# Kernel optimization log

Hardware: AMD Instinct MI355X
Metric: run time of the kernel (lower is better)

## Reference

```python
import jax, jax.numpy as jnp
import numpy as np
from jax import lax

NUM_EXPERTS = 5
K = 3


def setup_inputs() -> dict:
    key = jax.random.key(0)
    ks = jax.random.split(key, 16)
    B = 8192
    d_in, d_h = 32 * 10 * 10, 128

    def w(k, shape, fan_in):
        return jax.random.normal(k, shape, jnp.float32) / np.sqrt(fan_in)

    return {
        "x": jax.random.normal(ks[0], (B, 1, 28, 28), jnp.float32),
        # conv feature extractor: 28 -> conv5 -> 24 -> pool2 -> 12 -> conv3 -> 10
        "conv1_w": w(ks[1], (16, 1, 5, 5), 25),
        "conv1_b": jnp.zeros((16,), jnp.float32),
        "conv2_w": w(ks[2], (32, 16, 3, 3), 16 * 9),
        "conv2_b": jnp.zeros((32,), jnp.float32),
        # top-k gate
        "gate_w": w(ks[3], (d_in, NUM_EXPERTS), d_in),
        "gate_b": jnp.zeros((NUM_EXPERTS,), jnp.float32),
        # 5 experts: Linear(3200,128)-Tanh-Linear(128,128)-Tanh, stacked on axis 0
        "e1_w": w(ks[4], (NUM_EXPERTS, d_in, d_h), d_in),
        "e1_b": jnp.zeros((NUM_EXPERTS, d_h), jnp.float32),
        "e2_w": w(ks[5], (NUM_EXPERTS, d_h, d_h), d_h),
        "e2_b": jnp.zeros((NUM_EXPERTS, d_h), jnp.float32),
        # softmax head
        "sm_w": w(ks[6], (d_h, 10), d_h),
        "sm_b": jnp.zeros((10,), jnp.float32),
    }


def _conv_features(x, c1w, c1b, c2w, c2b):
    dn = ("NCHW", "OIHW", "NCHW")
    h = lax.conv_general_dilated(x, c1w, (1, 1), "VALID", dimension_numbers=dn)
    h = jax.nn.relu(h + c1b[None, :, None, None])          # [B,16,24,24]
    h = lax.reduce_window(h, -jnp.inf, lax.max, (1, 1, 2, 2), (1, 1, 2, 2), "VALID")  # [B,16,12,12]
    h = lax.conv_general_dilated(h, c2w, (1, 1), "VALID", dimension_numbers=dn)
    h = jax.nn.relu(h + c2b[None, :, None, None])          # [B,32,10,10]
    return h.reshape(h.shape[0], -1)                       # [B,3200]


def reference(x, conv1_w, conv1_b, conv2_w, conv2_b, gate_w, gate_b,
              e1_w, e1_b, e2_w, e2_b, sm_w, sm_b):
    h = _conv_features(x, conv1_w, conv1_b, conv2_w, conv2_b)  # [B, 3200]
    B = h.shape[0]

    # token-choice top-K gating over NUM_EXPERTS experts
    probs = jax.nn.softmax(h @ gate_w + gate_b, axis=-1)       # [B, E]
    topv, topi = lax.top_k(probs, K)                           # [B, K]
    topv = topv / jnp.sum(topv, axis=-1, keepdims=True)        # renormalize
    w_full = jnp.zeros((B, NUM_EXPERTS), h.dtype).at[
        jnp.arange(B)[:, None], topi].set(topv)                # [B, E] sparse combine weights

    # expert MLPs (small, computed densely and masked by gate weights)
    h1 = jnp.tanh(jnp.einsum("bd,edh->ebh", h, e1_w) + e1_b[:, None, :])   # [E,B,128]
    h2 = jnp.tanh(jnp.einsum("ebh,ehk->ebk", h1, e2_w) + e2_b[:, None, :])  # [E,B,128]
    moe_out = jnp.einsum("be,ebk->bk", w_full, h2)             # weighted sum combine, [B,128]

    logits = moe_out @ sm_w + sm_b                             # [B,10]
    return jax.nn.softmax(logits, axis=1)
```

## Files before the change

### kernel.cpp

```cpp
#include <hip/hip_runtime.h>
#include <hip/hip_bf16.h>
#include <hip/hip_fp16.h>

#define NB 8192
#define D_IN 3200
#define D_H 128
#define NE 5

typedef _Float16 f16x8 __attribute__((ext_vector_type(8)));
typedef _Float16 f16x4 __attribute__((ext_vector_type(4)));
typedef float f32x4 __attribute__((ext_vector_type(4)));

__device__ __forceinline__ void gload16(const _Float16* g, _Float16* l) {
    __builtin_amdgcn_global_load_lds(
        (const __attribute__((address_space(1))) void*)g,
        (__attribute__((address_space(3))) void*)l, 16, 0, 0);
}

__device__ __forceinline__ unsigned pack_hl(float v) {
    _Float16 vh = (_Float16)v;
    _Float16 vl = (_Float16)(v - (float)vh);
    unsigned short uh, ul;
    __builtin_memcpy(&uh, &vh, 2);
    __builtin_memcpy(&ul, &vl, 2);
    return (unsigned)uh | ((unsigned)ul << 16);
}

__global__ __launch_bounds__(256) void k_prep(const float* __restrict__ gw,
                                              const float* __restrict__ c2w,
                                              const float* __restrict__ c1w,
                                              float* __restrict__ gwC,
                                              _Float16* __restrict__ wpk,
                                              int* __restrict__ cnt) {
    int i = blockIdx.x * 256 + threadIdx.x;
    if (i < 16000) {
        int e = i / 3200, rem = i - e * 3200;
        int o = rem >> 5, co = rem & 31;
        gwC[i] = gw[(co * 100 + o) * 5 + e];
    } else if (i < 21120) {
        int j = i - 16000;
        int co = j / 160, k = j - co * 160;
        int s = k >> 4, ci = k & 15;
        float v = (s == 9) ? 0.f : c2w[(co * 16 + ci) * 9 + s];
        _Float16 vh = (_Float16)v;
        wpk[j] = vh;
        wpk[5120 + j] = (_Float16)(v - (float)vh);
    } else if (i < 21760) {
        int j = i - 21120;
        int c = (j * 1639) >> 16;
        int k = j - c * 40;
        float v = (k < 25) ? c1w[c * 25 + k] : 0.f;
        _Float16 vh = (_Float16)v;
        wpk[10240 + j] = vh;
        wpk[10880 + j] = (_Float16)(v - (float)vh);
    }
    if (blockIdx.x == 0 && threadIdx.x < NE) cnt[threadIdx.x] = 0;
}

#define PCL_S 24
__global__ __launch_bounds__(256, 4) void k_feat(
    const float* __restrict__ x, const float* __restrict__ c1b,
    const float* __restrict__ c2b,
    const float* __restrict__ gwC, const float* __restrict__ gb,
    const _Float16* __restrict__ wpk,
    const float* __restrict__ e1w, _Float16* __restrict__ wT,
    const float* __restrict__ e2w, _Float16* __restrict__ e2T,
    _Float16* __restrict__ h16, float* __restrict__ wfull)
{
    __shared__ union {
        struct {
            __align__(16) _Float16 b2h[5120];
            __align__(16) _Float16 b2l[5120];
            __align__(16) _Float16 b1h[640];
            __align__(16) _Float16 b1l[640];
            __align__(16) unsigned xs_hl[784];
            __align__(16) _Float16 pclh[144 * PCL_S];
            __align__(16) _Float16 pcll[144 * PCL_S];
            float red[32];
        } f;
        float tile[64 * 65];
    } S;
    int bid = blockIdx.x;
    int t = threadIdx.x;

    if (bid < 520) {
        if (bid < 500) {
            int e = bid / 100, rem = bid - e * 100;
            int k0 = (rem >> 1) * 64, n0 = (rem & 1) * 64;
            const float* src = e1w + (size_t)e * D_IN * D_H;
            _Float16* dst = wT + (size_t)e * D_H * D_IN;
            for (int i = 0; i < 16; ++i) {
                int idx = t + i * 256;
                int kr = idx >> 6, nc = idx & 63;
                S.tile[kr * 65 + nc] = src[(size_t)(k0 + kr) * D_H + n0 + nc];
            }
            __syncthreads();
            for (int i = 0; i < 16; ++i) {
                int idx = t + i * 256;
                int nr = idx >> 6, kc = idx & 63;
                dst[(size_t)(n0 + nr) * D_IN + k0 + kc] = (_Float16)S.tile[kc * 65 + nr];
            }
        } else {
            int idx2 = bid - 500;
            int e = idx2 >> 2, rem = idx2 & 3;
            int k0 = (rem >> 1) * 64, n0 = (rem & 1) * 64;
            const float* src = e2w + (size_t)e * D_H * D_H;
            _Float16* dst = e2T + (size_t)e * D_H * D_H;
            for (int i = 0; i < 16; ++i) {
                int idx = t + i * 256;
                int kr = idx >> 6, nc = idx & 63;
                S.tile[kr * 65 + nc] = src[(size_t)(k0 + kr) * D_H + n0 + nc];
            }
            __syncthreads();
            for (int i = 0; i < 16; ++i) {
                int idx = t + i * 256;
                int nr = idx >> 6, kc = idx & 63;
                dst[(size_t)(n0 + nr) * D_H + k0 + kc] = (_Float16)S.tile[kc * 65 + nr];
            }
        }
        return;
    }

    int b = bid - 520;
    int lane = t & 63, wv = t >> 6;
    int quad = lane >> 4, l16 = lane & 15;

    {
        _Float16* ldst = S.f.b2h;
        #pragma unroll
        for (int it = 0; it < 6; ++it) {
            int ci = t + it * 256;
            if (ci < 1440)
                gload16(wpk + ci * 8, ldst + (it * 256 + wv * 64) * 8);
        }
    }
    for (int i = t; i < 784; i += 256)
        S.f.xs_hl[i] = pack_hl(x[(size_t)b * 784 + i]);
    __syncthreads();

    {
        f16x8 b1hf = *(const f16x8*)&S.f.b1h[l16 * 40 + quad * 8];
        f16x8 b1lf = *(const f16x8*)&S.f.b1l[l16 * 40 + quad * 8];
        float bias1 = c1b[l16];
        int offw[8];
        #pragma unroll
        for (int j = 0; j < 8; ++j) {
            int k = quad * 8 + j; if (k > 24) k = 24;
            int uu = (k * 205) >> 10;
            offw[j] = k + 23 * uu;
        }
        int s_ = l16 & 3, qof = l16 >> 2;
        int dy = s_ >> 1, dx = s_ & 1;
        for (int T = wv * 9; T < wv * 9 + 9; ++T) {
            int q = T * 4 + qof;
            int qy = (q * 683) >> 13, qx = q - qy * 12;
            int base = (2 * qy + dy) * 28 + 2 * qx + dx;
            unsigned w[8];
            #pragma unroll
            for (int j = 0; j < 8; ++j) w[j] = S.f.xs_hl[base + offw[j]];
            union { f16x8 v; unsigned u[4]; } ah, al;
            #pragma unroll
            for (int jj = 0; jj < 4; ++jj) {
                ah.u[jj] = __builtin_amdgcn_perm(w[2 * jj + 1], w[2 * jj], 0x05040100u);
                al.u[jj] = __builtin_amdgcn_perm(w[2 * jj + 1], w[2 * jj], 0x07060302u);
            }
            f32x4 a1 = (f32x4){0.f, 0.f, 0.f, 0.f};
            a1 = __builtin_amdgcn_mfma_f32_16x16x32_f16(ah.v, b1hf, a1, 0, 0, 0);
            a1 = __builtin_amdgcn_mfma_f32_16x16x32_f16(ah.v, b1lf, a1, 0, 0, 0);
            a1 = __builtin_amdgcn_mfma_f32_16x16x32_f16(al.v, b1hf, a1, 0, 0, 0);
            float pv = fmaxf(fmaxf(a1[0], a1[1]), fmaxf(a1[2], a1[3]));
            pv = fmaxf(pv + bias1, 0.f);
            int pos = T * 4 + quad;
            _Float16 vh = (_Float16)pv;
            S.f.pclh[pos * PCL_S + l16] = vh;
            S.f.pcll[pos * PCL_S + l16] = (_Float16)(pv - (float)vh);
        }
    }
    __syncthreads();

    float part[5] = {0, 0, 0, 0, 0};
    int quadh = quad >> 1, quadl = quad & 1;
    const int offA[5] = {0, 2, 13, 24, 26};
    const int offB[5] = {1, 12, 14, 25, 0};
    {
        int nt = wv & 1;
        int co = nt * 16 + l16;
        f16x8 bh[5], bl[5];
        #pragma unroll
        for (int kc = 0; kc < 5; ++kc) {
            bh[kc] = *(const f16x8*)&S.f.b2h[co * 160 + kc * 32 + quad * 8];
            bl[kc] = *(const f16x8*)&S.f.b2l[co * 160 + kc * 32 + quad * 8];
        }
        float bco = c2b[co];
        for (int mt = wv >> 1; mt < 7; mt += 2) {
            int o_a = mt * 16 + l16;
            int o_cl = o_a < 100 ? o_a : 99;
            int pb = (o_cl / 10) * 12 + (o_cl % 10);
            f32x4 acc = (f32x4){0.f, 0.f, 0.f, 0.f};
            #pragma unroll
            for (int kc = 0; kc < 5; ++kc) {
                int off = quadh ? offB[kc] : offA[kc];
                f16x8 ah = *(const f16x8*)&S.f.pclh[(pb + off) * PCL_S + quadl * 8];
                f16x8 al = *(const f16x8*)&S.f.pcll[(pb + off) * PCL_S + quadl * 8];
                acc = __builtin_amdgcn_mfma_f32_16x16x32_f16(ah, bh[kc], acc, 0, 0, 0);
                acc = __builtin_amdgcn_mfma_f32_16x16x32_f16(ah, bl[kc], acc, 0, 0, 0);
                acc = __builtin_amdgcn_mfma_f32_16x16x32_f16(al, bh[kc], acc, 0, 0, 0);
            }
            if (mt < 6 || quad == 0) {
                int o0 = mt * 16 + quad * 4;
                f16x4 st;
                #pragma unroll
                for (int r = 0; r < 4; ++r) {
                    float hv = fmaxf(acc[r] + bco, 0.f);
                    st[r] = (_Float16)hv;
                    #pragma unroll
                    for (int e = 0; e < 5; ++e)
                        part[e] += hv * gwC[e * 3200 + (o0 + r) * 32 + co];
                }
                *(f16x4*)&h16[(size_t)b * D_IN + co * 100 + o0] = st;
            }
        }
    }

    #pragma unroll
    for (int e = 0; e < 5; ++e) {
        float v = part[e];
        for (int off = 32; off > 0; off >>= 1) v += __shfl_down(v, off, 64);
        if (lane == 0) S.f.red[wv * 8 + e] = v;
    }
    __syncthreads();
    if (t == 0) {
        float lg[5], p[5];
        float mx = -1e30f;
        for (int e = 0; e < 5; ++e) {
            lg[e] = S.f.red[e] + S.f.red[8 + e] + S.f.red[16 + e] + S.f.red[24 + e] + gb[e];
            mx = fmaxf(mx, lg[e]);
        }
        float sum = 0.f;
        for (int e = 0; e < 5; ++e) { p[e] = expf(lg[e] - mx); sum += p[e]; }
        for (int e = 0; e < 5; ++e) p[e] /= sum;
        bool used[5] = {false, false, false, false, false};
        float out5[5] = {0, 0, 0, 0, 0};
        int ti[3]; float tv[3]; float tsum = 0.f;
        for (int jj = 0; jj < 3; ++jj) {
            int best = 0; float bv = -1.f;
            for (int e = 0; e < 5; ++e)
                if (!used[e] && p[e] > bv) { bv = p[e]; best = e; }
            used[best] = true; ti[jj] = best; tv[jj] = bv; tsum += bv;
        }
        for (int jj = 0; jj < 3; ++jj) out5[ti[jj]] = tv[jj] / tsum;
        for (int e = 0; e < 5; ++e) wfull[b * 5 + e] = out5[e];
    }
}

__global__ __launch_bounds__(256) void k_compact(
    const float* __restrict__ wfull, int* __restrict__ cnt, int* __restrict__ lists)
{
    int tok = blockIdx.x * 256 + threadIdx.x;
    int lane = threadIdx.x & 63;
    float w[5];
    #pragma unroll
    for (int e = 0; e < 5; ++e) w[e] = wfull[(size_t)tok * 5 + e];
    #pragma unroll
    for (int e = 0; e < 5; ++e) {
        bool sel = w[e] > 0.f;
        unsigned long long mask = __ballot(sel);
        int leader = __ffsll((long long)mask) - 1;
        int base = 0;
        if (lane == leader) base = atomicAdd(&cnt[e], __popcll(mask));
        base = __shfl(base, leader, 64);
        if (sel) {
            int pos = base + __popcll(mask & ((1ull << lane) - 1ull));
            lists[e * NB + pos] = tok;
        }
    }
}

#define H1S 136
union __align__(16) SLds {
    struct { _Float16 As0[2048], As1[2048], Bs0[4096], Bs1[4096]; } p[2];
    struct {
        __align__(16) _Float16 h1s[64 * H1S];
        __align__(16) _Float16 e2ws[128 * H1S];
    } q;
};

__global__ __launch_bounds__(256, 3) void k_e1e2(
    const _Float16* __restrict__ h16, const _Float16* __restrict__ wT,
    const _Float16* __restrict__ e2T,
    const float* __restrict__ e1b, const float* __restrict__ e2b,
    const float* __restrict__ smw,
    const float* __restrict__ wfull, const int* __restrict__ cnt,
    const int* __restrict__ lists, float* __restrict__ logits)
{
    __shared__ SLds u;
    __shared__ float wfl[64];
    __shared__ int rows[64];
    int bid = blockIdx.x;
    int e = bid >> 7;
    int mt = bid & 127;
    int cnt_e = cnt[e];
    int m0 = mt * 64;
    if (m0 >= cnt_e) return;
    int t = threadIdx.x;
    int lane = t & 63, wv = t >> 6;
    int waveM = wv >> 1, waveN = wv & 1;
    int quad = lane >> 4, l16 = lane & 15;
    if (t < 64) {
        int r = m0 + t;
        int row = (r < cnt_e) ? lists[e * NB + r] : lists[e * NB];
        rows[t] = row;
        wfl[t] = (r < cnt_e) ? wfull[(size_t)row * 5 + e] : 0.f;
    }
    __syncthreads();

    const _Float16* bbase = wT + (size_t)e * (D_H * D_IN);
    int srow = t >> 2;
    int scol = (t & 3) * 8;
    const _Float16* aptr = h16 + (size_t)rows[srow] * D_IN + scol;
    const _Float16* bptr0 = bbase + (size_t)srow * D_IN + scol;
    const _Float16* bptr1 = bbase + (size_t)(64 + srow) * D_IN + scol;
    f32x4 acc[2][4];
    #pragma unroll
    for (int i = 0; i < 2; ++i)
        #pragma unroll
        for (int j = 0; j < 4; ++j) acc[i][j] = (f32x4){0.f, 0.f, 0.f, 0.f};

    _Float16* bufc = (_Float16*)&u.p[0];
    _Float16* bufn = (_Float16*)&u.p[1];
    #define STAGE(base, kk)                                           \
        do {                                                          \
            gload16(aptr  + (kk),        (base) + 0    + wv * 512);   \
            gload16(aptr  + (kk) + 32,   (base) + 2048 + wv * 512);   \
            gload16(bptr0 + (kk),        (base) + 4096 + wv * 512);   \
            gload16(bptr0 + (kk) + 32,   (base) + 8192 + wv * 512);   \
            gload16(bptr1 + (kk),        (base) + 4096 + 2048 + wv * 512); \
            gload16(bptr1 + (kk) + 32,   (base) + 8192 + 2048 + wv * 512); \
        } while (0)

    STAGE(bufc, 0);
    const int NT = D_IN / 64;
    for (int it = 0; it < NT; ++it) {
        if (it + 1 < NT) {
            STAGE(bufn, (it + 1) * 64);
            asm volatile("s_waitcnt vmcnt(6)" ::: "memory");
        } else {
            asm volatile("s_waitcnt vmcnt(0)" ::: "memory");
        }
        __builtin_amdgcn_s_barrier();
        __builtin_amdgcn_sched_barrier(0);
        #pragma unroll
        for (int ch = 0; ch < 2; ++ch) {
            const _Float16* Ab = bufc + (ch ? 2048 : 0);
            const _Float16* Bb = bufc + 4096 + (ch ? 4096 : 0);
            f16x8 af[2], bf[4];
            #pragma unroll
            for (int ms = 0; ms < 2; ++ms)
                af[ms] = *(const f16x8*)&Ab[(waveM * 32 + ms * 16 + l16) * 32 + quad * 8];
            #pragma unroll
            for (int ns = 0; ns < 4; ++ns)
                bf[ns] = *(const f16x8*)&Bb[(waveN * 64 + ns * 16 + l16) * 32 + quad * 8];
            #pragma unroll
            for (int ms = 0; ms < 2; ++ms)
                #pragma unroll
                for (int ns = 0; ns < 4; ++ns)
                    acc[ms][ns] = __builtin_amdgcn_mfma_f32_16x16x32_f16(af[ms], bf[ns], acc[ms][ns], 0, 0, 0);
        }
        __builtin_amdgcn_s_barrier();
        _Float16* tmp = bufc; bufc = bufn; bufn = tmp;
    }
    #undef STAGE

    #pragma unroll
    for (int ms = 0; ms < 2; ++ms) {
        int rbase = waveM * 32 + ms * 16 + quad * 4;
        #pragma unroll
        for (int ns = 0; ns < 4; ++ns) {
            int n = waveN * 64 + ns * 16 + l16;
            float bias = e1b[e * D_H + n];
            #pragma unroll
            for (int r = 0; r < 4; ++r)
                u.q.h1s[(rbase + r) * H1S + n] = (_Float16)tanhf(acc[ms][ns][r] + bias);
        }
    }
    __syncthreads();

    {
        int rr = t >> 1, cc = (t & 1) * 64;
        const _Float16* src = e2T + (size_t)e * (D_H * D_H) + (size_t)rr * D_H + cc;
        #pragma unroll
        for (int i = 0; i < 8; ++i)
            *(uint4*)&u.q.e2ws[rr * H1S + cc + i * 8] = *(const uint4*)(src + i * 8);
    }
    __syncthreads();

    f32x4 acc2[2][4];
    #pragma unroll
    for (int i = 0; i < 2; ++i)
        #pragma unroll
        for (int j = 0; j < 4; ++j) acc2[i][j] = (f32x4){0.f, 0.f, 0.f, 0.f};
    #pragma unroll
    for (int kc = 0; kc < 4; ++kc) {
        f16x8 a2[2], b2[4];
        #pragma unroll
        for (int ms = 0; ms < 2; ++ms)
            a2[ms] = *(const f16x8*)&u.q.h1s[(waveM * 32 + ms * 16 + l16) * H1S + kc * 32 + quad * 8];
        #pragma unroll
        for (int ns = 0; ns < 4; ++ns)
            b2[ns] = *(const f16x8*)&u.q.e2ws[(waveN * 64 + ns * 16 + l16) * H1S + kc * 32 + quad * 8];
        #pragma unroll
        for (int ms = 0; ms < 2; ++ms)
            #pragma unroll
            for (int ns = 0; ns < 4; ++ns)
                acc2[ms][ns] = __builtin_amdgcn_mfma_f32_16x16x32_f16(a2[ms], b2[ns], acc2[ms][ns], 0, 0, 0);
    }
    __syncthreads();

    _Float16* smwT = u.q.e2ws;
    for (int i = t; i < 2048; i += 256) {
        int n = i >> 7, k = i & 127;
        smwT[i] = (_Float16)(n < 10 ? smw[k * 10 + n] : 0.f);
    }
    #pragma unroll
    for (int ms = 0; ms < 2; ++ms) {
        int rbase = waveM * 32 + ms * 16 + quad * 4;
        #pragma unroll
        for (int ns = 0; ns < 4; ++ns) {
            int n = waveN * 64 + ns * 16 + l16;
            float bias = e2b[e * D_H + n];
            #pragma unroll
            for (int r = 0; r < 4; ++r) {
                int lrow = rbase + r;
                u.q.h1s[lrow * H1S + n] = (_Float16)(wfl[lrow] * tanhf(acc2[ms][ns][r] + bias));
            }
        }
    }
    __syncthreads();

    {
        f32x4 acc3 = (f32x4){0.f, 0.f, 0.f, 0.f};
        #pragma unroll
        for (int kc = 0; kc < 4; ++kc) {
            f16x8 a3 = *(const f16x8*)&u.q.h1s[(wv * 16 + l16) * H1S + kc * 32 + quad * 8];
            f16x8 b3 = *(const f16x8*)&smwT[l16 * 128 + kc * 32 + quad * 8];
            acc3 = __builtin_amdgcn_mfma_f32_16x16x32_f16(a3, b3, acc3, 0, 0, 0);
        }
        if (l16 < 10) {
            #pragma unroll
            for (int r = 0; r < 4; ++r) {
                int row = wv * 16 + quad * 4 + r;
                unsafeAtomicAdd(&logits[(size_t)rows[row] * 10 + l16], acc3[r]);
            }
        }
    }
}

__global__ __launch_bounds__(256) void k_smax(
    const float* __restrict__ logits, const float* __restrict__ smb,
    float* __restrict__ out)
{
    int r = blockIdx.x * 256 + threadIdx.x;
    float lg[10];
    float mx = -1e30f;
    #pragma unroll
    for (int c = 0; c < 10; ++c) {
        lg[c] = logits[(size_t)r * 10 + c] + smb[c];
        mx = fmaxf(mx, lg[c]);
    }
    float s = 0.f;
    #pragma unroll
    for (int c = 0; c < 10; ++c) { lg[c] = expf(lg[c] - mx); s += lg[c]; }
    float inv = 1.f / s;
    #pragma unroll
    for (int c = 0; c < 10; ++c) out[(size_t)r * 10 + c] = lg[c] * inv;
}

extern "C" void kernel_launch(void* const* d_in, const int* in_sizes, int n_in,
                              void* d_out, int out_size, void* d_ws, size_t ws_size,
                              hipStream_t stream)
{
    const float* x   = (const float*)d_in[0];
    const float* c1w = (const float*)d_in[1];
    const float* c1b = (const float*)d_in[2];
    const float* c2w = (const float*)d_in[3];
    const float* c2b = (const float*)d_in[4];
    const float* gw  = (const float*)d_in[5];
    const float* gb  = (const float*)d_in[6];
    const float* e1w = (const float*)d_in[7];
    const float* e1b = (const float*)d_in[8];
    const float* e2w = (const float*)d_in[9];
    const float* e2b = (const float*)d_in[10];
    const float* smw = (const float*)d_in[11];
    const float* smb = (const float*)d_in[12];
    float* out = (float*)d_out;

    char* ws = (char*)d_ws;
    size_t off = 0;
    auto alloc = [&](size_t bytes) {
        void* p = ws + off;
        off += (bytes + 255) & ~(size_t)255;
        return p;
    };
    _Float16* h16 = (_Float16*)alloc((size_t)NB * D_IN * 2);
    _Float16* wT  = (_Float16*)alloc((size_t)NE * D_H * D_IN * 2);
    _Float16* e2T = (_Float16*)alloc((size_t)NE * D_H * D_H * 2);
    float* wfull  = (float*)alloc((size_t)NB * NE * 4);
    float* logits = (float*)alloc((size_t)NB * 10 * 4);
    float* gwC    = (float*)alloc((size_t)NE * D_IN * 4);
    _Float16* wpk = (_Float16*)alloc((size_t)11520 * 2);
    int* cnt      = (int*)alloc(NE * 4);
    int* lists    = (int*)alloc((size_t)NE * NB * 4);

    hipMemsetAsync(logits, 0, (size_t)NB * 10 * 4, stream);
    k_prep<<<dim3(85), 256, 0, stream>>>(gw, c2w, c1w, gwC, wpk, cnt);
    k_feat<<<dim3(520 + NB), 256, 0, stream>>>(x, c1b, c2b, gwC, gb, wpk,
                                               e1w, wT, e2w, e2T, h16, wfull);
    k_compact<<<dim3(NB / 256), 256, 0, stream>>>(wfull, cnt, lists);
    k_e1e2<<<dim3(128 * NE), 256, 0, stream>>>(h16, wT, e2T, e1b, e2b, smw,
                                               wfull, cnt, lists, logits);
    k_smax<<<dim3(NB / 256), 256, 0, stream>>>(logits, smb, out);
}
```

Before: 264.1 us.

## Pad conv2 LDS weights, interleave gate weights per expert, vectorize input staging

Gate weights are repacked into an 8-wide interleaved layout so each output element reads its five expert gate weights with one vector load plus one scalar load, instead of five strided scalar loads. The conv2 weight rows in LDS are padded from 160 to 168 halves to reduce bank conflicts. Conv1 weights are now read from global memory rather than staged in LDS, which shrinks the LDS copy. The input image is loaded as float4 and packed four values per thread. In exchange the gate-weight buffer grows and conv1 weights now come through the cache instead of LDS.

```diff
diff --git a/kernel.cpp b/kernel.cpp
--- a/kernel.cpp
+++ b/kernel.cpp
@@ -29,30 +29,30 @@
 __global__ __launch_bounds__(256) void k_prep(const float* __restrict__ gw,
                                               const float* __restrict__ c2w,
                                               const float* __restrict__ c1w,
-                                              float* __restrict__ gwC,
+                                              float* __restrict__ gwC8,
                                               _Float16* __restrict__ wpk,
                                               int* __restrict__ cnt) {
     int i = blockIdx.x * 256 + threadIdx.x;
-    if (i < 16000) {
-        int e = i / 3200, rem = i - e * 3200;
-        int o = rem >> 5, co = rem & 31;
-        gwC[i] = gw[(co * 100 + o) * 5 + e];
-    } else if (i < 21120) {
-        int j = i - 16000;
+    if (i < 25600) {
+        int idx = i >> 3, e = i & 7;
+        int o = idx >> 5, co = idx & 31;
+        gwC8[i] = (e < 5) ? gw[(co * 100 + o) * 5 + e] : 0.f;
+    } else if (i < 30720) {
+        int j = i - 25600;
         int co = j / 160, k = j - co * 160;
         int s = k >> 4, ci = k & 15;
         float v = (s == 9) ? 0.f : c2w[(co * 16 + ci) * 9 + s];
         _Float16 vh = (_Float16)v;
-        wpk[j] = vh;
-        wpk[5120 + j] = (_Float16)(v - (float)vh);
-    } else if (i < 21760) {
-        int j = i - 21120;
+        wpk[co * 168 + k] = vh;
+        wpk[5376 + co * 168 + k] = (_Float16)(v - (float)vh);
+    } else if (i < 31360) {
+        int j = i - 30720;
         int c = (j * 1639) >> 16;
         int k = j - c * 40;
         float v = (k < 25) ? c1w[c * 25 + k] : 0.f;
         _Float16 vh = (_Float16)v;
-        wpk[10240 + j] = vh;
-        wpk[10880 + j] = (_Float16)(v - (float)vh);
+        wpk[10752 + j] = vh;
+        wpk[11392 + j] = (_Float16)(v - (float)vh);
     }
     if (blockIdx.x == 0 && threadIdx.x < NE) cnt[threadIdx.x] = 0;
 }
@@ -61,7 +61,7 @@
 __global__ __launch_bounds__(256, 4) void k_feat(
     const float* __restrict__ x, const float* __restrict__ c1b,
     const float* __restrict__ c2b,
-    const float* __restrict__ gwC, const float* __restrict__ gb,
+    const float* __restrict__ gwC8, const float* __restrict__ gb,
     const _Float16* __restrict__ wpk,
     const float* __restrict__ e1w, _Float16* __restrict__ wT,
     const float* __restrict__ e2w, _Float16* __restrict__ e2T,
@@ -69,10 +69,8 @@
 {
     __shared__ union {
         struct {
-            __align__(16) _Float16 b2h[5120];
-            __align__(16) _Float16 b2l[5120];
-            __align__(16) _Float16 b1h[640];
-            __align__(16) _Float16 b1l[640];
+            __align__(16) _Float16 b2h[5376];
+            __align__(16) _Float16 b2l[5376];
             __align__(16) unsigned xs_hl[784];
             __align__(16) _Float16 pclh[144 * PCL_S];
             __align__(16) _Float16 pcll[144 * PCL_S];
@@ -130,17 +128,22 @@
         #pragma unroll
         for (int it = 0; it < 6; ++it) {
             int ci = t + it * 256;
-            if (ci < 1440)
+            if (ci < 1344)
                 gload16(wpk + ci * 8, ldst + (it * 256 + wv * 64) * 8);
         }
     }
-    for (int i = t; i < 784; i += 256)
-        S.f.xs_hl[i] = pack_hl(x[(size_t)b * 784 + i]);
+    if (t < 196) {
+        float4 v4 = *(const float4*)&x[(size_t)b * 784 + t * 4];
+        uint4 pk;
+        pk.x = pack_hl(v4.x); pk.y = pack_hl(v4.y);
+        pk.z = pack_hl(v4.z); pk.w = pack_hl(v4.w);
+        *(uint4*)&S.f.xs_hl[t * 4] = pk;
+    }
     __syncthreads();
 
     {
-        f16x8 b1hf = *(const f16x8*)&S.f.b1h[l16 * 40 + quad * 8];
-        f16x8 b1lf = *(const f16x8*)&S.f.b1l[l16 * 40 + quad * 8];
+        f16x8 b1hf = *(const f16x8*)&wpk[10752 + l16 * 40 + quad * 8];
+        f16x8 b1lf = *(const f16x8*)&wpk[11392 + l16 * 40 + quad * 8];
         float bias1 = c1b[l16];
         int offw[8];
         #pragma unroll
@@ -188,8 +191,8 @@
         f16x8 bh[5], bl[5];
         #pragma unroll
         for (int kc = 0; kc < 5; ++kc) {
-            bh[kc] = *(const f16x8*)&S.f.b2h[co * 160 + kc * 32 + quad * 8];
-            bl[kc] = *(const f16x8*)&S.f.b2l[co * 160 + kc * 32 + quad * 8];
+            bh[kc] = *(const f16x8*)&S.f.b2h[co * 168 + kc * 32 + quad * 8];
+            bl[kc] = *(const f16x8*)&S.f.b2l[co * 168 + kc * 32 + quad * 8];
         }
         float bco = c2b[co];
         for (int mt = wv >> 1; mt < 7; mt += 2) {
@@ -213,9 +216,13 @@
                 for (int r = 0; r < 4; ++r) {
                     float hv = fmaxf(acc[r] + bco, 0.f);
                     st[r] = (_Float16)hv;
-                    #pragma unroll
-                    for (int e = 0; e < 5; ++e)
-                        part[e] += hv * gwC[e * 3200 + (o0 + r) * 32 + co];
+                    int idx = (o0 + r) * 32 + co;
+                    const f32x4 g0 = *(const f32x4*)&gwC8[(size_t)idx * 8];
+                    part[0] += hv * g0[0];
+                    part[1] += hv * g0[1];
+                    part[2] += hv * g0[2];
+                    part[3] += hv * g0[3];
+                    part[4] += hv * gwC8[(size_t)idx * 8 + 4];
                 }
                 *(f16x4*)&h16[(size_t)b * D_IN + co * 100 + o0] = st;
             }
@@ -506,14 +513,14 @@
     _Float16* e2T = (_Float16*)alloc((size_t)NE * D_H * D_H * 2);
     float* wfull  = (float*)alloc((size_t)NB * NE * 4);
     float* logits = (float*)alloc((size_t)NB * 10 * 4);
-    float* gwC    = (float*)alloc((size_t)NE * D_IN * 4);
-    _Float16* wpk = (_Float16*)alloc((size_t)11520 * 2);
+    float* gwC8   = (float*)alloc((size_t)25600 * 4);
+    _Float16* wpk = (_Float16*)alloc((size_t)12032 * 2);
     int* cnt      = (int*)alloc(NE * 4);
     int* lists    = (int*)alloc((size_t)NE * NB * 4);
 
     hipMemsetAsync(logits, 0, (size_t)NB * 10 * 4, stream);
-    k_prep<<<dim3(85), 256, 0, stream>>>(gw, c2w, c1w, gwC, wpk, cnt);
-    k_feat<<<dim3(520 + NB), 256, 0, stream>>>(x, c1b, c2b, gwC, gb, wpk,
+    k_prep<<<dim3(123), 256, 0, stream>>>(gw, c2w, c1w, gwC8, wpk, cnt);
+    k_feat<<<dim3(520 + NB), 256, 0, stream>>>(x, c1b, c2b, gwC8, gb, wpk,
                                                e1w, wT, e2w, e2T, h16, wfull);
     k_compact<<<dim3(NB / 256), 256, 0, stream>>>(wfull, cnt, lists);
     k_e1e2<<<dim3(128 * NE), 256, 0, stream>>>(h16, wT, e2T, e1b, e2b, smw,
```

After: 270.2 us. 2.3% more time.

## Triple-buffer expert-1 GEMM loads and read expert-2 weights from global

Applied to the files above, without the earlier changes.

The K-loop of the expert-1 GEMM moves from a double-buffered to a triple-buffered LDS pipeline. Two stages are now in flight and the wait allows twelve outstanding loads, which hides more global latency. To make room in LDS, the expert-2 weight tile is no longer staged in LDS; its MFMA operands are read directly from global memory. Launch bounds drop from 3 to 2 blocks per CU because the LDS footprint grows, so the deeper pipeline costs occupancy.

```diff
diff --git a/kernel.cpp b/kernel.cpp
--- a/kernel.cpp
+++ b/kernel.cpp
@@ -278,14 +278,14 @@
 
 #define H1S 136
 union __align__(16) SLds {
-    struct { _Float16 As0[2048], As1[2048], Bs0[4096], Bs1[4096]; } p[2];
+    struct { _Float16 d[12288]; } p[3];
     struct {
         __align__(16) _Float16 h1s[64 * H1S];
-        __align__(16) _Float16 e2ws[128 * H1S];
+        __align__(16) _Float16 smwT[2048];
     } q;
 };
 
-__global__ __launch_bounds__(256, 3) void k_e1e2(
+__global__ __launch_bounds__(256, 2) void k_e1e2(
     const _Float16* __restrict__ h16, const _Float16* __restrict__ wT,
     const _Float16* __restrict__ e2T,
     const float* __restrict__ e1b, const float* __restrict__ e2b,
@@ -326,8 +326,9 @@
         #pragma unroll
         for (int j = 0; j < 4; ++j) acc[i][j] = (f32x4){0.f, 0.f, 0.f, 0.f};
 
-    _Float16* bufc = (_Float16*)&u.p[0];
-    _Float16* bufn = (_Float16*)&u.p[1];
+    _Float16* bcur = (_Float16*)&u.p[0];
+    _Float16* bnxt = (_Float16*)&u.p[1];
+    _Float16* bnx2 = (_Float16*)&u.p[2];
     #define STAGE(base, kk)                                           \
         do {                                                          \
             gload16(aptr  + (kk),        (base) + 0    + wv * 512);   \
@@ -338,11 +339,14 @@
             gload16(bptr1 + (kk) + 32,   (base) + 8192 + 2048 + wv * 512); \
         } while (0)
 
-    STAGE(bufc, 0);
+    STAGE(bcur, 0);
+    STAGE(bnxt, 64);
     const int NT = D_IN / 64;
     for (int it = 0; it < NT; ++it) {
-        if (it + 1 < NT) {
-            STAGE(bufn, (it + 1) * 64);
+        if (it + 2 < NT) {
+            STAGE(bnx2, (it + 2) * 64);
+            asm volatile("s_waitcnt vmcnt(12)" ::: "memory");
+        } else if (it + 1 < NT) {
             asm volatile("s_waitcnt vmcnt(6)" ::: "memory");
         } else {
             asm volatile("s_waitcnt vmcnt(0)" ::: "memory");
@@ -351,8 +355,8 @@
         __builtin_amdgcn_sched_barrier(0);
         #pragma unroll
         for (int ch = 0; ch < 2; ++ch) {
-            const _Float16* Ab = bufc + (ch ? 2048 : 0);
-            const _Float16* Bb = bufc + 4096 + (ch ? 4096 : 0);
+            const _Float16* Ab = bcur + (ch ? 2048 : 0);
+            const _Float16* Bb = bcur + 4096 + (ch ? 4096 : 0);
             f16x8 af[2], bf[4];
             #pragma unroll
             for (int ms = 0; ms < 2; ++ms)
@@ -367,7 +371,7 @@
                     acc[ms][ns] = __builtin_amdgcn_mfma_f32_16x16x32_f16(af[ms], bf[ns], acc[ms][ns], 0, 0, 0);
         }
         __builtin_amdgcn_s_barrier();
-        _Float16* tmp = bufc; bufc = bufn; bufn = tmp;
+        _Float16* t0 = bcur; bcur = bnxt; bnxt = bnx2; bnx2 = t0;
     }
     #undef STAGE
 
@@ -385,15 +389,7 @@
     }
     __syncthreads();
 
-    {
-        int rr = t >> 1, cc = (t & 1) * 64;
-        const _Float16* src = e2T + (size_t)e * (D_H * D_H) + (size_t)rr * D_H + cc;
-        #pragma unroll
-        for (int i = 0; i < 8; ++i)
-            *(uint4*)&u.q.e2ws[rr * H1S + cc + i * 8] = *(const uint4*)(src + i * 8);
-    }
-    __syncthreads();
-
+    const _Float16* e2g = e2T + (size_t)e * (D_H * D_H);
     f32x4 acc2[2][4];
     #pragma unroll
     for (int i = 0; i < 2; ++i)
@@ -407,7 +403,7 @@
             a2[ms] = *(const f16x8*)&u.q.h1s[(waveM * 32 + ms * 16 + l16) * H1S + kc * 32 + quad * 8];
         #pragma unroll
         for (int ns = 0; ns < 4; ++ns)
-            b2[ns] = *(const f16x8*)&u.q.e2ws[(waveN * 64 + ns * 16 + l16) * H1S + kc * 32 + quad * 8];
+            b2[ns] = *(const f16x8*)&e2g[(size_t)(waveN * 64 + ns * 16 + l16) * D_H + kc * 32 + quad * 8];
         #pragma unroll
         for (int ms = 0; ms < 2; ++ms)
             #pragma unroll
@@ -416,7 +412,7 @@
     }
     __syncthreads();
 
-    _Float16* smwT = u.q.e2ws;
+    _Float16* smwT = u.q.smwT;
     for (int i = t; i < 2048; i += 256) {
         int n = i >> 7, k = i & 127;
         smwT[i] = (_Float16)(n < 10 ? smw[k * 10 + n] : 0.f);
```

Result: faster. 251.8 us, median of 2 (-4.7%).
